# Performance work log

Measured on AMD Instinct MI355X. Metric: run time of the kernel, lower is better.

Reference implementation:

```python
import jax, jax.numpy as jnp
import numpy as np

B, M = 2, 8192          # clouds per batch, points per cloud (N = B*M)
K_NEAR, K_FAR, K_SMOOTH = 8, 16, 8
T_LOC, T_CON = 0.1, 0.5
EPS = 1e-8


def setup_inputs() -> dict:
    key = jax.random.key(0)
    k1, k2 = jax.random.split(key)
    scores = jax.random.uniform(k1, (B * M,), dtype=jnp.float32)          # in [0,1]
    coords = jax.random.normal(k2, (B * M, 3), dtype=jnp.float32) * 2.0   # point positions
    batch_ids = (jnp.arange(B * M, dtype=jnp.int32) // M).astype(jnp.int32)
    return {"scores": scores, "coords": coords, "batch_ids": batch_ids}


def _knn_global(coords):
    """Per-cloud brute-force kNN (self included as first neighbor, like pointops.knn_query).
    coords: (N,3) -> global indices (N, K_FAR)."""
    c = coords.reshape(B, M, 3)

    def per_cloud(cb):  # cb: (M,3)
        sq = jnp.sum(cb * cb, axis=-1)                      # (M,)
        d2 = sq[:, None] + sq[None, :] - 2.0 * (cb @ cb.T)  # (M,M) squared dists
        _, idx = jax.lax.top_k(-d2, K_FAR)                  # (M,K_FAR) smallest dists
        return idx

    idx = jax.vmap(per_cloud)(c)                            # (B,M,K_FAR) local indices
    idx = idx + (jnp.arange(B, dtype=idx.dtype) * M)[:, None, None]
    return idx.reshape(B * M, K_FAR)


def _loss_terms(scores, coords, idx):
    # --- locality: neighbors (incl. self) should have similar scores ---
    nb = idx[:, :K_NEAR]                                    # (N,k)
    score_diff = jnp.abs(scores[:, None] - scores[nb])      # (N,k)
    dists = jnp.linalg.norm(coords[:, None, :] - coords[nb], axis=2)  # (N,k)
    w = jnp.exp(-dists / T_LOC)
    loss_loc = jnp.sum(w * score_diff ** 2) / jnp.clip(jnp.sum(w), 1e-8)

    # --- contrastive: near similar, far dissimilar ---
    sim_pos = 1.0 - jnp.abs(scores[:, None] - scores[idx[:, :K_NEAR]])
    sim_neg = 1.0 - jnp.abs(scores[:, None] - scores[idx[:, K_NEAR:K_FAR]])
    loss_pos = -jnp.mean(jnp.log(jax.nn.sigmoid(sim_pos / T_CON) + EPS))
    loss_neg = -jnp.mean(jnp.log(1.0 - jax.nn.sigmoid(sim_neg / T_CON) + EPS))
    loss_con = loss_pos + loss_neg

    # --- distribution: sorted scores match uniform linspace per cloud ---
    sb = jnp.sort(scores.reshape(B, M), axis=1)             # (B,M)
    target = jnp.linspace(0.0, 1.0, M, dtype=scores.dtype)  # (M,)
    loss_dist = jnp.mean(jnp.mean((sb - target[None, :]) ** 2, axis=1))

    # --- smoothness: score close to neighbor mean ---
    nmean = jnp.mean(scores[idx[:, :K_SMOOTH]], axis=1)     # (N,)
    loss_smooth = jnp.mean((scores - nmean) ** 2)

    return loss_loc, loss_con, loss_dist, loss_smooth


def reference(scores, coords, batch_ids):
    del batch_ids  # equal-sized clouds; batch structure is (B, M) by construction
    idx = _knn_global(coords)
    l_loc, l_con, l_dist, l_smooth = _loss_terms(scores, coords, idx)
    total = 1.0 * l_loc + 0.5 * l_con + 0.3 * l_dist + 0.2 * l_smooth
    return total
```

## Files before the change

kernel.cpp:

```cpp
#include <hip/hip_runtime.h>
#include <math.h>

#define BB 2
#define MM 8192
#define NN (BB * MM)
#define NBATCH (NN / 16)
#define NCELL 4096
#define LOSS_BLOCKS 1024

#define PART_OFF   0
#define RANK_OFF   24576
#define IDX_OFF    90112
#define PK_OFF     1138688
#define SS_OFF     1400832
#define CELLID_OFF 1466368
#define CNT_OFF    1531904
#define CUR_OFF    1564672
#define BBLO_OFF   1597440
#define BBHI_OFF   1613824
#define DONE_OFF   1630208

__device__ __forceinline__ unsigned mort3(unsigned x, unsigned y, unsigned z) {
    unsigned m = 0;
#pragma unroll
    for (int i = 0; i < 4; ++i) {
        m |= ((x >> i) & 1u) << (3 * i);
        m |= ((y >> i) & 1u) << (3 * i + 1);
        m |= ((z >> i) & 1u) << (3 * i + 2);
    }
    return m;
}

__global__ __launch_bounds__(1024) void prepA_kernel(
    const float* __restrict__ coords, int* __restrict__ cellid,
    int* __restrict__ cursor, unsigned* __restrict__ done) {
    __shared__ int hist[NCELL];
    __shared__ int wsum[16];
    const int tid = threadIdx.x, blk = blockIdx.x;
    const int pbase = blk * MM;
    for (int i = tid; i < NCELL; i += 1024) hist[i] = 0;
    if (blk == 0 && tid == 0) *done = 0u;
    __syncthreads();

#pragma unroll
    for (int it = 0; it < 8; ++it) {
        const int i = pbase + it * 1024 + tid;
        float x = coords[3 * i], y = coords[3 * i + 1], z = coords[3 * i + 2];
        int cx = min(15, max(0, (int)floorf(x) + 8));
        int cy = min(15, max(0, (int)floorf(y) + 8));
        int cz = min(15, max(0, (int)floorf(z) + 8));
        const int c = (int)mort3((unsigned)cx, (unsigned)cy, (unsigned)cz);
        cellid[i] = blk * NCELL + c;
        atomicAdd(&hist[c], 1);
    }
    __syncthreads();

    int v[4]; int run = 0;
#pragma unroll
    for (int i = 0; i < 4; ++i) { int t = hist[tid * 4 + i]; v[i] = run; run += t; }
    const int lane = tid & 63, wv = tid >> 6;
    int inc = run;
#pragma unroll
    for (int off = 1; off < 64; off <<= 1) {
        int y = __shfl_up(inc, off);
        if (lane >= off) inc += y;
    }
    int laneExcl = inc - run;
    if (lane == 63) wsum[wv] = inc;
    __syncthreads();
    int wbase = 0;
#pragma unroll
    for (int w = 0; w < 16; ++w) wbase += (w < wv) ? wsum[w] : 0;
    const int base = wbase + laneExcl;
#pragma unroll
    for (int i = 0; i < 4; ++i)
        cursor[blk * NCELL + tid * 4 + i] = pbase + base + v[i];
}

__global__ void scatter_kernel(const float* __restrict__ coords, const float* __restrict__ scores,
                               const int* __restrict__ cellid, int* __restrict__ cursor,
                               float4* __restrict__ pk_s, float* __restrict__ s_s) {
    int i = blockIdx.x * 256 + threadIdx.x;
    if (i < NN) {
        int pos = atomicAdd(&cursor[cellid[i]], 1);
        float x = coords[3 * i], y = coords[3 * i + 1], z = coords[3 * i + 2];
        float sq = fmaf(x, x, fmaf(y, y, z * z));
        pk_s[pos] = make_float4(x, y, z, sq);
        s_s[pos] = scores[i];
    }
}

__global__ void bbox_kernel(const float4* __restrict__ pk_s, float4* __restrict__ bb_lo,
                            float4* __restrict__ bb_hi) {
    int b = blockIdx.x * 256 + threadIdx.x;
    if (b < NBATCH) {
        float4 c = pk_s[b * 16];
        float lx = c.x, ly = c.y, lz = c.z, hx = c.x, hy = c.y, hz = c.z;
#pragma unroll
        for (int i = 1; i < 16; ++i) {
            c = pk_s[b * 16 + i];
            lx = fminf(lx, c.x); ly = fminf(ly, c.y); lz = fminf(lz, c.z);
            hx = fmaxf(hx, c.x); hy = fmaxf(hy, c.y); hz = fmaxf(hz, c.z);
        }
        bb_lo[b] = make_float4(lx, ly, lz, 0.f);
        bb_hi[b] = make_float4(hx, hy, hz, 0.f);
    }
}

__device__ __forceinline__ void sort16(unsigned (&a)[16]) {
#pragma unroll
    for (int p2 = 1; p2 < 16; p2 <<= 1) {
#pragma unroll
        for (int k2 = p2; k2 >= 1; k2 >>= 1) {
#pragma unroll
            for (int j2 = k2 % p2; j2 + k2 < 16; j2 += 2 * k2) {
#pragma unroll
                for (int i2 = 0; i2 < k2; ++i2) {
                    if (i2 + j2 + k2 < 16) {
                        if (((i2 + j2) / (2 * p2)) == ((i2 + j2 + k2) / (2 * p2))) {
                            unsigned x = a[i2 + j2], y = a[i2 + j2 + k2];
                            a[i2 + j2]      = min(x, y);
                            a[i2 + j2 + k2] = max(x, y);
                        }
                    }
                }
            }
        }
    }
}

__device__ __forceinline__ void truncmerge(unsigned (&slot)[16], const unsigned (&kb)[16]) {
    unsigned m[16];
#pragma unroll
    for (int k = 0; k < 16; ++k) m[k] = min(slot[k], kb[15 - k]);
#pragma unroll
    for (int st = 8; st >= 1; st >>= 1) {
#pragma unroll
        for (int i = 0; i < 16; ++i) {
            if ((i & st) == 0) {
                unsigned lo = min(m[i], m[i + st]);
                unsigned hi = max(m[i], m[i + st]);
                m[i] = lo; m[i + st] = hi;
            }
        }
    }
#pragma unroll
    for (int k = 0; k < 16; ++k) slot[k] = m[k];
}

__global__ __launch_bounds__(1024) void knnrank_kernel(const float4* __restrict__ pk_s,
                                                       const float* __restrict__ s_s,
                                                       const float4* __restrict__ bb_lo,
                                                       const float4* __restrict__ bb_hi,
                                                       int* __restrict__ out_idx,
                                                       int* __restrict__ out_rank) {
    __shared__ unsigned lds_k[16][16][64];
    __shared__ int lds_aux[16][64];
    __shared__ unsigned lds_tmin[64];
    const int tid = threadIdx.x, lane = tid & 63;
    const int wv = __builtin_amdgcn_readfirstlane(tid >> 6);

    if (blockIdx.x >= 256) {
        const int qbase = (blockIdx.x - 256) << 6;
        const int cloudbase = (qbase >> 13) << 13;
        const float s = s_s[qbase + lane];
        const float* __restrict__ sc = s_s + cloudbase;
        int rk = 0;
        const int j0 = wv * 512;
        for (int jj = 0; jj < 512; jj += 16) {
#pragma unroll
            for (int i = 0; i < 16; ++i) {
                rk += (sc[j0 + jj + i] < s) ? 1 : 0;
            }
        }
        lds_aux[wv][lane] = rk;
        __syncthreads();
        if (wv == 0) {
            int rsum = 0;
#pragma unroll
            for (int w = 0; w < 16; ++w) rsum += lds_aux[w][lane];
            out_rank[qbase + lane] = rsum;
        }
        return;
    }

    const int qbase = blockIdx.x * 64;
    const int cloudbase = (qbase >> 13) << 13;
    const float4 p = pk_s[qbase + lane];
    const int sb0 = (qbase - cloudbase) >> 4;
    const float4* __restrict__ pc = pk_s + cloudbase;
    const int bbase = cloudbase >> 4;

    if (tid < 64) lds_tmin[tid] = 0x7f7fffffu;

    unsigned slot[16];
#pragma unroll
    for (int k = 0; k < 16; ++k) slot[k] = 0x7F000000u + (unsigned)k;
    float t_f = 3.0e38f;

    auto batch = [&](int bi) {
        unsigned kb[16];
#pragma unroll
        for (int i = 0; i < 16; ++i) {
            const int j = bi * 16 + i;
            const float4 c = pc[j];
            float dot = fmaf(p.x, c.x, fmaf(p.y, c.y, p.z * c.z));
            float d2  = fmaf(-2.0f, dot, p.w + c.w);
            kb[i] = (__float_as_uint(d2) & 0xFFFFE000u) | (unsigned)j;
        }
        sort16(kb);
        truncmerge(slot, kb);
        const unsigned nt = (slot[15] & 0xFFFFE000u) + 0x2000u;
        const float ntf = __uint_as_float(nt);
        if (ntf < t_f) {
            t_f = ntf;
            atomicMin(&lds_tmin[lane], nt);
        }
    };

    const int r = sb0 & 15;
    const int ownb = (wv >= r && wv < r + 4) ? (sb0 + (wv - r)) : -1;
    __syncthreads();
    if (ownb >= 0) batch(ownb);
    lds_aux[wv][lane] = (int)__float_as_uint(t_f);
    __syncthreads();
    float tb = __uint_as_float((unsigned)lds_aux[0][lane]);
#pragma unroll
    for (int w = 1; w < 16; ++w) tb = fminf(tb, __uint_as_float((unsigned)lds_aux[w][lane]));
    t_f = fminf(t_f, tb);

    float4 lo = bb_lo[bbase + wv];
    float4 hi = bb_hi[bbase + wv];
    for (int k = 0; k < 32; ++k) {
        const int bi = wv + (k << 4);
        float4 lo_n, hi_n;
        if (k + 1 < 32) {
            lo_n = bb_lo[bbase + bi + 16];
            hi_n = bb_hi[bbase + bi + 16];
        }
        if (bi != ownb) {
            const unsigned tmb = *((volatile unsigned*)&lds_tmin[lane]);
            const float tsh = fminf(t_f, __uint_as_float(tmb));
            float dx = fmaxf(fmaxf(lo.x - p.x, p.x - hi.x), 0.f);
            float dy = fmaxf(fmaxf(lo.y - p.y, p.y - hi.y), 0.f);
            float dz = fmaxf(fmaxf(lo.z - p.z, p.z - hi.z), 0.f);
            float lb = fmaf(dx, dx, fmaf(dy, dy, dz * dz));
            if (__any(fmaf(lb, 0.999f, -1e-5f) < tsh)) batch(bi);
        }
        lo = lo_n; hi = hi_n;
    }

#pragma unroll
    for (int k = 0; k < 16; ++k) lds_k[wv][k][lane] = slot[k];

    for (int half = 8; half >= 1; half >>= 1) {
        __syncthreads();
        if (wv < half) {
            unsigned a[16], m[16];
#pragma unroll
            for (int k = 0; k < 16; ++k) a[k] = lds_k[wv][k][lane];
#pragma unroll
            for (int k = 0; k < 16; ++k) m[k] = min(a[k], lds_k[wv + half][15 - k][lane]);
#pragma unroll
            for (int st = 8; st >= 1; st >>= 1) {
#pragma unroll
                for (int i = 0; i < 16; ++i) {
                    if ((i & st) == 0) {
                        unsigned lo2 = min(m[i], m[i + st]);
                        unsigned hi2 = max(m[i], m[i + st]);
                        m[i] = lo2; m[i + st] = hi2;
                    }
                }
            }
#pragma unroll
            for (int k = 0; k < 16; ++k) lds_k[wv][k][lane] = m[k];
        }
    }
    __syncthreads();

    if (wv == 0) {
#pragma unroll
        for (int k = 0; k < 16; ++k)
            out_idx[(qbase + lane) * 16 + k] = (int)(lds_k[0][k][lane] & 0x1FFFu) + cloudbase;
    }
}

__global__ __launch_bounds__(256) void lossfin_kernel(const float* __restrict__ s_s,
                                                      const float4* __restrict__ pk_s,
                                                      const int* __restrict__ knn,
                                                      const int* __restrict__ rnk,
                                                      float* __restrict__ partial,
                                                      unsigned* __restrict__ done,
                                                      float* __restrict__ out) {
    __shared__ float red[4][6];
    __shared__ float sgrp[16][6];
    __shared__ unsigned lastflag;
    const int t = blockIdx.x * 256 + threadIdx.x;
    const int q = t >> 4, k = t & 15;
    const int nb = knn[t];
    const float s  = s_s[q];
    const float sn = s_s[nb];
    const float diff = fabsf(s - sn);
    const float sim = 1.0f - diff;
    const float sg = 1.0f / (1.0f + expf(-2.0f * sim));

    float a_wd = 0.f, a_w = 0.f, a_pos = 0.f, a_neg = 0.f, snk = 0.f;
    if (k < 8) {
        float4 pq = pk_s[q];
        float4 pn = pk_s[nb];
        float dx = pq.x - pn.x, dy = pq.y - pn.y, dz = pq.z - pn.z;
        float d = sqrtf(dx * dx + dy * dy + dz * dz);
        float w = expf(-10.0f * d);
        a_wd = w * diff * diff;
        a_w  = w;
        a_pos = logf(sg + 1e-8f);
        snk = sn;
    } else {
        a_neg = logf(1.0f - sg + 1e-8f);
    }

    float nsum = snk;
#pragma unroll
    for (int off = 1; off < 16; off <<= 1) nsum += __shfl_xor(nsum, off);

    float a_sm = 0.f, a_di = 0.f;
    if (k == 0) {
        float t1 = s - nsum * 0.125f;
        a_sm = t1 * t1;
        float t2 = s - (float)rnk[q] * (1.0f / 8191.0f);
        a_di = t2 * t2;
    }

#pragma unroll
    for (int off = 1; off < 64; off <<= 1) {
        a_wd  += __shfl_xor(a_wd, off);
        a_w   += __shfl_xor(a_w, off);
        a_pos += __shfl_xor(a_pos, off);
        a_neg += __shfl_xor(a_neg, off);
        a_sm  += __shfl_xor(a_sm, off);
        a_di  += __shfl_xor(a_di, off);
    }
    const int wv = threadIdx.x >> 6;
    if ((threadIdx.x & 63) == 0) {
        red[wv][0] = a_wd; red[wv][1] = a_w; red[wv][2] = a_pos;
        red[wv][3] = a_neg; red[wv][4] = a_sm; red[wv][5] = a_di;
    }
    __syncthreads();
    if (threadIdx.x < 6) {
        float v = red[0][threadIdx.x] + red[1][threadIdx.x] +
                  red[2][threadIdx.x] + red[3][threadIdx.x];
        __hip_atomic_store(&partial[threadIdx.x * LOSS_BLOCKS + blockIdx.x], v,
                           __ATOMIC_RELEASE, __HIP_MEMORY_SCOPE_AGENT);
    }
    __syncthreads();
    if (threadIdx.x == 0)
        lastflag = __hip_atomic_fetch_add(done, 1u, __ATOMIC_ACQ_REL, __HIP_MEMORY_SCOPE_AGENT);
    __syncthreads();

    if (lastflag == (unsigned)(LOSS_BLOCKS - 1)) {
        const int tid = threadIdx.x, lane2 = tid & 63, w4 = tid >> 6;
#pragma unroll
        for (int rep = 0; rep < 4; ++rep) {
            const int w = w4 * 4 + rep;
            float a[6];
#pragma unroll
            for (int term = 0; term < 6; ++term)
                a[term] = __hip_atomic_load(&partial[term * LOSS_BLOCKS + w * 64 + lane2],
                                            __ATOMIC_ACQUIRE, __HIP_MEMORY_SCOPE_AGENT);
#pragma unroll
            for (int off = 1; off < 64; off <<= 1) {
#pragma unroll
                for (int term = 0; term < 6; ++term) a[term] += __shfl_xor(a[term], off);
            }
            if (lane2 == 0) {
#pragma unroll
                for (int term = 0; term < 6; ++term) sgrp[w][term] = a[term];
            }
        }
        __syncthreads();
        if (tid == 0) {
            float acc[6];
#pragma unroll
            for (int term = 0; term < 6; ++term) {
                float v = 0.f;
#pragma unroll
                for (int w = 0; w < 16; ++w) v += sgrp[w][term];
                acc[term] = v;
            }
            float l_loc = acc[0] / fmaxf(acc[1], 1e-8f);
            float l_pos = -acc[2] / (float)(NN * 8);
            float l_neg = -acc[3] / (float)(NN * 8);
            float l_sm  = acc[4] / (float)NN;
            float l_di  = acc[5] / (float)NN;
            out[0] = l_loc + 0.5f * (l_pos + l_neg) + 0.3f * l_di + 0.2f * l_sm;
        }
    }
}

extern "C" void kernel_launch(void* const* d_in, const int* in_sizes, int n_in,
                              void* d_out, int out_size, void* d_ws, size_t ws_size,
                              hipStream_t stream) {
    const float* scores = (const float*)d_in[0];
    const float* coords = (const float*)d_in[1];
    (void)in_sizes; (void)n_in; (void)out_size; (void)ws_size;

    char* ws = (char*)d_ws;
    float*  part  = (float*)(ws + PART_OFF);
    int*    rank  = (int*)(ws + RANK_OFF);
    int*    knn   = (int*)(ws + IDX_OFF);
    float4* pk_s  = (float4*)(ws + PK_OFF);
    float*  s_s   = (float*)(ws + SS_OFF);
    int*    cellid= (int*)(ws + CELLID_OFF);
    int*    cursor= (int*)(ws + CUR_OFF);
    float4* bb_lo = (float4*)(ws + BBLO_OFF);
    float4* bb_hi = (float4*)(ws + BBHI_OFF);
    unsigned* done= (unsigned*)(ws + DONE_OFF);
    float*  out   = (float*)d_out;

    prepA_kernel<<<2, 1024, 0, stream>>>(coords, cellid, cursor, done);
    scatter_kernel<<<64, 256, 0, stream>>>(coords, scores, cellid, cursor, pk_s, s_s);
    bbox_kernel<<<4, 256, 0, stream>>>(pk_s, bb_lo, bb_hi);
    knnrank_kernel<<<512, 1024, 0, stream>>>(pk_s, s_s, bb_lo, bb_hi, knn, rank);
    lossfin_kernel<<<LOSS_BLOCKS, 256, 0, stream>>>(s_s, pk_s, knn, rank, part, done, out);
}
```

Baseline: 159.8 us.

## Split kNN candidate scan into two half-cloud blocks per query group and merge

Each 64-query group's candidate scan is split across two blocks, each covering half of the cloud's 512 batches, doubling the knn block count from 256 to 512. Each block writes its partial top-16 keys to a workspace buffer, and a new merge2 kernel combines the two lists and writes the final indices. The block that does not own the query's own batches still sorts them to seed its pruning threshold. The aim is more parallelism on the GPU's many CUs, at the cost of an extra kernel launch, extra global traffic and weaker pruning in the far half.

```diff
diff --git a/kernel.cpp b/kernel.cpp
--- a/kernel.cpp
+++ b/kernel.cpp
@@ -14,11 +14,11 @@
 #define PK_OFF     1138688
 #define SS_OFF     1400832
 #define CELLID_OFF 1466368
-#define CNT_OFF    1531904
 #define CUR_OFF    1564672
 #define BBLO_OFF   1597440
 #define BBHI_OFF   1613824
 #define DONE_OFF   1630208
+#define PKEY_OFF   1634304
 
 __device__ __forceinline__ unsigned mort3(unsigned x, unsigned y, unsigned z) {
     unsigned m = 0;
@@ -152,7 +152,7 @@
                                                        const float* __restrict__ s_s,
                                                        const float4* __restrict__ bb_lo,
                                                        const float4* __restrict__ bb_hi,
-                                                       int* __restrict__ out_idx,
+                                                       unsigned* __restrict__ pkeys,
                                                        int* __restrict__ out_rank) {
     __shared__ unsigned lds_k[16][16][64];
     __shared__ int lds_aux[16][64];
@@ -160,8 +160,8 @@
     const int tid = threadIdx.x, lane = tid & 63;
     const int wv = __builtin_amdgcn_readfirstlane(tid >> 6);
 
-    if (blockIdx.x >= 256) {
-        const int qbase = (blockIdx.x - 256) << 6;
+    if (blockIdx.x >= 512) {
+        const int qbase = (blockIdx.x - 512) << 6;
         const int cloudbase = (qbase >> 13) << 13;
         const float s = s_s[qbase + lane];
         const float* __restrict__ sc = s_s + cloudbase;
@@ -184,12 +184,16 @@
         return;
     }
 
-    const int qbase = blockIdx.x * 64;
+    const int g = blockIdx.x >> 1;
+    const int h = blockIdx.x & 1;
+    const int qbase = g << 6;
     const int cloudbase = (qbase >> 13) << 13;
     const float4 p = pk_s[qbase + lane];
     const int sb0 = (qbase - cloudbase) >> 4;
     const float4* __restrict__ pc = pk_s + cloudbase;
     const int bbase = cloudbase >> 4;
+    const int hb0 = h << 8;
+    const int hs = sb0 >> 8;
 
     if (tid < 64) lds_tmin[tid] = 0x7f7fffffu;
 
@@ -198,8 +202,7 @@
     for (int k = 0; k < 16; ++k) slot[k] = 0x7F000000u + (unsigned)k;
     float t_f = 3.0e38f;
 
-    auto batch = [&](int bi) {
-        unsigned kb[16];
+    auto loadkeys = [&](int bi, unsigned (&kb)[16]) {
 #pragma unroll
         for (int i = 0; i < 16; ++i) {
             const int j = bi * 16 + i;
@@ -208,6 +211,11 @@
             float d2  = fmaf(-2.0f, dot, p.w + c.w);
             kb[i] = (__float_as_uint(d2) & 0xFFFFE000u) | (unsigned)j;
         }
+    };
+
+    auto batch = [&](int bi) {
+        unsigned kb[16];
+        loadkeys(bi, kb);
         sort16(kb);
         truncmerge(slot, kb);
         const unsigned nt = (slot[15] & 0xFFFFE000u) + 0x2000u;
@@ -221,7 +229,18 @@
     const int r = sb0 & 15;
     const int ownb = (wv >= r && wv < r + 4) ? (sb0 + (wv - r)) : -1;
     __syncthreads();
-    if (ownb >= 0) batch(ownb);
+    if (ownb >= 0) {
+        if (h == hs) {
+            batch(ownb);
+        } else {
+            unsigned kb[16];
+            loadkeys(ownb, kb);
+            sort16(kb);
+            const unsigned nt = (kb[15] & 0xFFFFE000u) + 0x2000u;
+            t_f = fminf(t_f, __uint_as_float(nt));
+            atomicMin(&lds_tmin[lane], nt);
+        }
+    }
     lds_aux[wv][lane] = (int)__float_as_uint(t_f);
     __syncthreads();
     float tb = __uint_as_float((unsigned)lds_aux[0][lane]);
@@ -229,16 +248,16 @@
     for (int w = 1; w < 16; ++w) tb = fminf(tb, __uint_as_float((unsigned)lds_aux[w][lane]));
     t_f = fminf(t_f, tb);
 
-    float4 lo = bb_lo[bbase + wv];
-    float4 hi = bb_hi[bbase + wv];
-    for (int k = 0; k < 32; ++k) {
-        const int bi = wv + (k << 4);
+    float4 lo = bb_lo[bbase + hb0 + wv];
+    float4 hi = bb_hi[bbase + hb0 + wv];
+    for (int k = 0; k < 16; ++k) {
+        const int bi = hb0 + wv + (k << 4);
         float4 lo_n, hi_n;
-        if (k + 1 < 32) {
+        if (k + 1 < 16) {
             lo_n = bb_lo[bbase + bi + 16];
             hi_n = bb_hi[bbase + bi + 16];
         }
-        if (bi != ownb) {
+        if (bi != ownb || h != hs) {
             const unsigned tmb = *((volatile unsigned*)&lds_tmin[lane]);
             const float tsh = fminf(t_f, __uint_as_float(tmb));
             float dx = fmaxf(fmaxf(lo.x - p.x, p.x - hi.x), 0.f);
@@ -281,8 +300,24 @@
     if (wv == 0) {
 #pragma unroll
         for (int k = 0; k < 16; ++k)
-            out_idx[(qbase + lane) * 16 + k] = (int)(lds_k[0][k][lane] & 0x1FFFu) + cloudbase;
-    }
+            pkeys[(unsigned)(blockIdx.x * 16 + k) * 64 + lane] = lds_k[0][k][lane];
+    }
+}
+
+__global__ __launch_bounds__(256) void merge2_kernel(const unsigned* __restrict__ pkeys,
+                                                     int* __restrict__ out_idx) {
+    const int t = blockIdx.x * 256 + threadIdx.x;
+    const int g = t >> 6, lane = t & 63;
+    const int cloudbase = (g >> 7) << 13;
+    unsigned a[16], b[16];
+#pragma unroll
+    for (int k = 0; k < 16; ++k) a[k] = pkeys[(unsigned)((g * 2 + 0) * 16 + k) * 64 + lane];
+#pragma unroll
+    for (int k = 0; k < 16; ++k) b[k] = pkeys[(unsigned)((g * 2 + 1) * 16 + k) * 64 + lane];
+    truncmerge(a, b);
+#pragma unroll
+    for (int k = 0; k < 16; ++k)
+        out_idx[(g * 64 + lane) * 16 + k] = (int)(a[k] & 0x1FFFu) + cloudbase;
 }
 
 __global__ __launch_bounds__(256) void lossfin_kernel(const float* __restrict__ s_s,
@@ -415,11 +450,13 @@
     float4* bb_lo = (float4*)(ws + BBLO_OFF);
     float4* bb_hi = (float4*)(ws + BBHI_OFF);
     unsigned* done= (unsigned*)(ws + DONE_OFF);
+    unsigned* pkeys = (unsigned*)(ws + PKEY_OFF);
     float*  out   = (float*)d_out;
 
     prepA_kernel<<<2, 1024, 0, stream>>>(coords, cellid, cursor, done);
     scatter_kernel<<<64, 256, 0, stream>>>(coords, scores, cellid, cursor, pk_s, s_s);
     bbox_kernel<<<4, 256, 0, stream>>>(pk_s, bb_lo, bb_hi);
-    knnrank_kernel<<<512, 1024, 0, stream>>>(pk_s, s_s, bb_lo, bb_hi, knn, rank);
+    knnrank_kernel<<<768, 1024, 0, stream>>>(pk_s, s_s, bb_lo, bb_hi, pkeys, rank);
+    merge2_kernel<<<64, 256, 0, stream>>>(pkeys, knn);
     lossfin_kernel<<<LOSS_BLOCKS, 256, 0, stream>>>(s_s, pk_s, knn, rank, part, done, out);
 }
```

Result: slower. 165.7 us (+3.7%).
